# Optimization experiments

Measured on AMD Instinct MI355X. Metric: run time of the kernel, lower is better.

Reference implementation:

```python
import jax, jax.numpy as jnp
import numpy as np


def _gelu(x):
    return jax.nn.gelu(x, approximate=False)


def _mlp(g, w1, b1, w2, b2, w3, b3):
    # MLP1D: Linear(1,64) -> GELU -> Linear(64,64) -> GELU -> Linear(64,R)
    h = _gelu(g[:, None] @ w1.T + b1)
    h = _gelu(h @ w2.T + b2)
    return h @ w3.T + b3


def _forward(x,
             ah_w1, ah_b1, ah_w2, ah_b2, ah_w3, ah_b3,
             bc1_w1, bc1_b1, bc1_w2, bc1_b2, bc1_w3, bc1_b3,
             aw_w1, aw_b1, aw_w2, aw_b2, aw_w3, aw_b3,
             bc2_w1, bc2_b1, bc2_w2, bc2_b2, bc2_w3, bc2_b3,
             ca_w1, ca_b1, ca_dw, ca_db, lc_w, bn_g, bn_b, bn_m, bn_v):
    B, C, H, W = x.shape
    C2 = C // 2
    R = ah_w3.shape[0]
    xh, xw = jnp.split(x, 2, axis=1)  # (B, C2, H, W) each

    # normalized rFFT half-spectrum coordinates in [-1, 1]
    omega_h = (2.0 * jnp.pi * jnp.arange(H // 2 + 1, dtype=jnp.float32) / H) / jnp.pi - 1.0
    omega_w = (2.0 * jnp.pi * jnp.arange(W // 2 + 1, dtype=jnp.float32) / W) / jnp.pi - 1.0
    lam = jnp.linspace(-1.0, 1.0, C2, dtype=jnp.float32)

    # outer-product gates (band=None -> no mask)
    Ah = _mlp(omega_h, ah_w1, ah_b1, ah_w2, ah_b2, ah_w3, ah_b3)      # (Hh, R)
    Bh = _mlp(lam, bc1_w1, bc1_b1, bc1_w2, bc1_b2, bc1_w3, bc1_b3)    # (C2, R)
    Gh = jax.nn.softplus(jnp.einsum('hr,cr->hc', Ah, Bh)) / jnp.sqrt(jnp.float32(R))
    Aw = _mlp(omega_w, aw_w1, aw_b1, aw_w2, aw_b2, aw_w3, aw_b3)      # (Wh, R)
    Bw = _mlp(lam, bc2_w1, bc2_b1, bc2_w2, bc2_b2, bc2_w3, bc2_b3)    # (C2, R)
    Gw = jax.nn.softplus(jnp.einsum('wr,cr->wc', Aw, Bw)) / jnp.sqrt(jnp.float32(R))

    # HC branch: rFFT along H, gate (C2, Hh), irFFT (ChannelBasis is identity)
    zh = jnp.fft.rfft(xh, axis=2, norm='ortho') * Gh.T[None, :, :, None]
    yh = jnp.fft.irfft(zh, n=H, axis=2, norm='ortho')
    # WC branch: rFFT along W, gate (C2, Wh)
    zw = jnp.fft.rfft(xw, axis=3, norm='ortho') * Gw.T[None, :, None, :]
    yw = jnp.fft.irfft(zw, n=W, axis=3, norm='ortho')
    y = jnp.concatenate([yh, yw], axis=1)  # (B, C, H, W)

    # ChannelAttentionBlock: gap -> 1x1 conv -> GELU -> dw 3x3 -> sigmoid * y
    p = jnp.mean(y, axis=(2, 3))                        # (B, C)
    p = _gelu(p @ ca_w1.T + ca_b1)
    # depthwise 3x3 with padding=1 on a 1x1 spatial map == center tap only
    p = p * ca_dw[:, 1, 1][None, :] + ca_db[None, :]
    y = jax.nn.sigmoid(p)[:, :, None, None] * y

    # SimpleConv: 1x1 conv (no bias) -> BatchNorm (eval) -> GELU
    y = jnp.einsum('oc,bchw->bohw', lc_w, y)
    inv = bn_g / jnp.sqrt(bn_v + 1e-5)
    y = _gelu(y * inv[None, :, None, None] + (bn_b - bn_m * inv)[None, :, None, None])
    return x + y


def setup_inputs() -> dict:
    key = jax.random.key(0)
    ks = iter(jax.random.split(key, 48))
    B, C, H, W = 4, 256, 256, 256
    R, HID = 8, 64

    def lin(o, i):
        return jax.random.normal(next(ks), (o, i), jnp.float32) / np.sqrt(i).astype(np.float32)

    def vec(n):
        return jax.random.normal(next(ks), (n,), jnp.float32) * 0.02

    d = {"x": jax.random.normal(next(ks), (B, C, H, W), jnp.float32)}
    for name in ["ah", "bc1", "aw", "bc2"]:
        d[f"{name}_w1"] = lin(HID, 1)
        d[f"{name}_b1"] = vec(HID)
        d[f"{name}_w2"] = lin(HID, HID)
        d[f"{name}_b2"] = vec(HID)
        d[f"{name}_w3"] = lin(R, HID)
        d[f"{name}_b3"] = vec(R)
    d["ca_w1"] = lin(C, C)
    d["ca_b1"] = vec(C)
    d["ca_dw"] = jax.random.normal(next(ks), (C, 3, 3), jnp.float32) / 3.0
    d["ca_db"] = vec(C)
    d["lc_w"] = lin(C, C)
    d["bn_g"] = jnp.ones((C,), jnp.float32)
    d["bn_b"] = jnp.zeros((C,), jnp.float32)
    d["bn_m"] = vec(C)
    d["bn_v"] = jnp.ones((C,), jnp.float32)
    return d


def reference(x,
              ah_w1, ah_b1, ah_w2, ah_b2, ah_w3, ah_b3,
              bc1_w1, bc1_b1, bc1_w2, bc1_b2, bc1_w3, bc1_b3,
              aw_w1, aw_b1, aw_w2, aw_b2, aw_w3, aw_b3,
              bc2_w1, bc2_b1, bc2_w2, bc2_b2, bc2_w3, bc2_b3,
              ca_w1, ca_b1, ca_dw, ca_db, lc_w, bn_g, bn_b, bn_m, bn_v):
    return _forward(x,
                    ah_w1, ah_b1, ah_w2, ah_b2, ah_w3, ah_b3,
                    bc1_w1, bc1_b1, bc1_w2, bc1_b2, bc1_w3, bc1_b3,
                    aw_w1, aw_b1, aw_w2, aw_b2, aw_w3, aw_b3,
                    bc2_w1, bc2_b1, bc2_w2, bc2_b2, bc2_w3, bc2_b3,
                    ca_w1, ca_b1, ca_dw, ca_db, lc_w, bn_g, bn_b, bn_m, bn_v)
```

## Files before the change

### kernel.cpp

```cpp
#include <hip/hip_runtime.h>
#include <math.h>

#define DEV __device__ __forceinline__

typedef __attribute__((ext_vector_type(8))) short short8;
typedef __attribute__((ext_vector_type(4))) float floatx4;
typedef unsigned int u32;
typedef unsigned short u16;

DEV float gelu_f(float v) { return 0.5f * v * (1.0f + erff(v * 0.70710678118654752f)); }
DEV float softplus_f(float v) { return v > 15.0f ? v : log1pf(expf(v)); }

DEV u16 f2bf(float v) {
    u32 u = __float_as_uint(v);
    return (u16)((u + 0x7fffu + ((u >> 16) & 1u)) >> 16);
}

DEV void gload_lds16(const void* g, void* l) {
    __builtin_amdgcn_global_load_lds((const __attribute__((address_space(1))) u32*)g,
                                     (__attribute__((address_space(3))) u32*)l, 16, 0, 0);
}

#define WS_A(j)     ((j) * 1040)
#define WS_KBUF     4160
#define WS_P        (4160 + 65536)
#define WS_S        (WS_P + 1024)
#define Y0_B        286976u
#define AW0_B       134504704u
#define CIRC0_B     135028992u
#define XB0_B       168583424u
#define YT0_B       135028992u

struct MlpW { const float *w1, *b1, *w2, *b2, *w3, *b3; };

__global__ void mlp_kernel(MlpW a0, MlpW a1, MlpW a2, MlpW a3, float* ws) {
    int j = blockIdx.x;
    MlpW m = (j == 0) ? a0 : (j == 1) ? a1 : (j == 2) ? a2 : a3;
    int n = (j == 1 || j == 3) ? 128 : 129;
    int i = threadIdx.x;
    if (i >= n) return;
    float g;
    if (j == 1 || j == 3) g = -1.0f + 2.0f * i / 127.0f;
    else                  g = 2.0f * i / 256.0f - 1.0f;
    float h1[64], h2[64];
    for (int k = 0; k < 64; k++) h1[k] = gelu_f(g * m.w1[k] + m.b1[k]);
    for (int q = 0; q < 64; q++) {
        float acc = m.b2[q];
        for (int k = 0; k < 64; k++) acc += h1[k] * m.w2[q * 64 + k];
        h2[q] = gelu_f(acc);
    }
    float* outp = ws + WS_A(j) + i * 8;
    for (int r = 0; r < 8; r++) {
        float acc = m.b3[r];
        for (int k = 0; k < 64; k++) acc += h2[k] * m.w3[r * 64 + k];
        outp[r] = acc;
    }
}

__global__ void gatek_kernel(float* ws) {
    int br = blockIdx.x >> 7, c = blockIdx.x & 127;
    const float* A = ws + WS_A(br == 0 ? 0 : 2);
    const float* B = ws + WS_A(br == 0 ? 1 : 3);
    __shared__ float G[129];
    int t = threadIdx.x;
    if (t < 129) {
        float acc = 0.f;
        for (int r = 0; r < 8; r++) acc += A[t * 8 + r] * B[c * 8 + r];
        G[t] = softplus_f(acc) * 0.35355339059327373f;
    }
    __syncthreads();
    float g0 = G[0], g128 = G[128];
    float acc = g0 + ((t & 1) ? -g128 : g128);
    for (int f = 1; f < 128; f++) {
        int idx = (f * t) & 255;
        acc += 2.0f * G[f] * cosf(idx * 0.02454369260617026f);
    }
    ws[WS_KBUF + blockIdx.x * 256 + t] = acc * (1.0f / 256.0f);
}

__global__ void circmat(const float* __restrict__ ws, u16* __restrict__ circ) {
    int mi = blockIdx.x, t = threadIdx.x;
    __shared__ float kl[256];
    kl[t] = ws[WS_KBUF + mi * 256 + t];
    __syncthreads();
    u16* M = circ + (size_t)mi * 65536u;
    for (int it = 0; it < 32; it++) {
        int e = it * 2048 + t * 8;
        int i = e >> 8, j = e & 255;
        u16 tmp[8];
#pragma unroll
        for (int jj = 0; jj < 8; jj++) tmp[jj] = f2bf(kl[(i - j - jj) & 255]);
        *(uint4*)&M[e] = *(uint4*)tmp;
    }
}

__global__ void prep(const float* __restrict__ x, u16* __restrict__ xb) {
    int tile = blockIdx.x;
    int mat = blockIdx.y;
    int t = threadIdx.x;
    const float* xm = x + (size_t)mat * 65536u;
    u16* xo = xb + (size_t)mat * 65536u;
    __shared__ float lt[64][65];
    if ((mat & 255) >= 128) {
        int base = tile * 4096 + t * 16;
#pragma unroll
        for (int q = 0; q < 4; q++) {
            float4 v = *(const float4*)&xm[base + q * 4];
            ushort4 o; o.x = f2bf(v.x); o.y = f2bf(v.y); o.z = f2bf(v.z); o.w = f2bf(v.w);
            *(ushort4*)&xo[base + q * 4] = o;
        }
    } else {
        int w0 = (tile & 3) * 64, h0 = (tile >> 2) * 64;
        int rh = t >> 2, cc = (t & 3) * 16;
#pragma unroll
        for (int q = 0; q < 4; q++) {
            float4 v = *(const float4*)&xm[(h0 + rh) * 256 + w0 + cc + q * 4];
            lt[rh][cc + q * 4 + 0] = v.x; lt[rh][cc + q * 4 + 1] = v.y;
            lt[rh][cc + q * 4 + 2] = v.z; lt[rh][cc + q * 4 + 3] = v.w;
        }
        __syncthreads();
        u16 tmp[16];
#pragma unroll
        for (int j = 0; j < 16; j++) tmp[j] = f2bf(lt[cc + j][rh]);
#pragma unroll
        for (int q = 0; q < 4; q++)
            *(ushort4*)&xo[(w0 + rh) * 256 + h0 + cc + q * 4] = *(ushort4*)&tmp[q * 4];
    }
}

__global__ __launch_bounds__(256) void gate_gemm(
    const u16* __restrict__ xb, const u16* __restrict__ circ,
    u16* __restrict__ y, float* __restrict__ ws)
{
    const int tile = blockIdx.x, c = blockIdx.y, zb = blockIdx.z;
    const int b = zb >> 1, br = zb & 1;
    const int m0 = (tile >> 1) * 128, n0 = (tile & 1) * 128;
    const int t = threadIdx.x, lane = t & 63, w = t >> 6;
    const int ch = br * 128 + c;

    const u16* Mbase = circ + (size_t)ch * 65536u;
    const u16* Xbase = xb + (size_t)(b * 256 + ch) * 65536u;
    const int rM0 = br ? n0 : m0;
    const int rX0 = br ? m0 : n0;

    __shared__ u16 ldsM[4096];
    __shared__ u16 ldsX[4096];

    const int s1 = t + 256;
    const int kq0 = t >> 7, r0s = t & 127;
    const int kq1 = s1 >> 7, r1s = s1 & 127;
    const u16* gM0 = Mbase + (rM0 + r0s) * 256 + kq0 * 8;
    const u16* gM1 = Mbase + (rM0 + r1s) * 256 + kq1 * 8;
    const u16* gX0 = Xbase + (rX0 + r0s) * 256 + kq0 * 8;
    const u16* gX1 = Xbase + (rX0 + r1s) * 256 + kq1 * 8;
    u16* lM0 = &ldsM[(t & 192) * 8];
    u16* lM1 = &ldsM[((t & 192) + 256) * 8];
    u16* lX0 = &ldsX[(t & 192) * 8];
    u16* lX1 = &ldsX[((t & 192) + 256) * 8];

    floatx4 acc[4][4];
#pragma unroll
    for (int i = 0; i < 4; i++)
#pragma unroll
        for (int j = 0; j < 4; j++) acc[i][j] = (floatx4){0.f, 0.f, 0.f, 0.f};

    const int wm = (w & 1) * 64, wn = (w >> 1) * 64;
    const int fr = lane & 15, fq = lane >> 4;
    const u16* aB = br ? ldsX : ldsM;
    const u16* bB = br ? ldsM : ldsX;

    for (int k0 = 0; k0 < 256; k0 += 32) {
        gload_lds16(gM0, lM0); gload_lds16(gM1, lM1);
        gload_lds16(gX0, lX0); gload_lds16(gX1, lX1);
        gM0 += 32; gM1 += 32; gX0 += 32; gX1 += 32;
        __syncthreads();
        short8 aF[4], bF[4];
#pragma unroll
        for (int i = 0; i < 4; i++) aF[i] = *(const short8*)&aB[(fq * 128 + wm + i * 16 + fr) * 8];
#pragma unroll
        for (int j = 0; j < 4; j++) bF[j] = *(const short8*)&bB[(fq * 128 + wn + j * 16 + fr) * 8];
#pragma unroll
        for (int i = 0; i < 4; i++)
#pragma unroll
            for (int j = 0; j < 4; j++)
                acc[i][j] = __builtin_amdgcn_mfma_f32_16x16x32_bf16(aF[i], bF[j], acc[i][j], 0, 0, 0);
        __syncthreads();
    }

    size_t ybase = (size_t)(b * 256 + ch) * 65536u;
    float lsum = 0.f;
#pragma unroll
    for (int i = 0; i < 4; i++)
#pragma unroll
        for (int r = 0; r < 4; r++) {
            int row = m0 + wm + i * 16 + fq * 4 + r;
            size_t rb = ybase + (size_t)row * 256;
#pragma unroll
            for (int j = 0; j < 4; j++) {
                float v = acc[i][j][r];
                lsum += v;
                y[rb + n0 + wn + j * 16 + fr] = f2bf(v);
            }
        }
    for (int off = 32; off; off >>= 1) lsum += __shfl_down(lsum, off, 64);
    __shared__ float wsum[4];
    if (lane == 0) wsum[w] = lsum;
    __syncthreads();
    if (t == 0) atomicAdd(ws + WS_P + b * 256 + ch, wsum[0] + wsum[1] + wsum[2] + wsum[3]);
}

__global__ void attn_kernel(const float* __restrict__ ca_w1, const float* __restrict__ ca_b1,
                            const float* __restrict__ ca_dw, const float* __restrict__ ca_db,
                            const float* __restrict__ lc_w, float* ws, u16* __restrict__ aw) {
    int b = blockIdx.x, o = threadIdx.x;
    __shared__ float pm[256];
    __shared__ float sl[256];
    pm[o] = ws[WS_P + b * 256 + o] * (1.0f / 65536.0f);
    __syncthreads();
    float acc = ca_b1[o];
    for (int c2 = 0; c2 < 256; c2++) acc += ca_w1[o * 256 + c2] * pm[c2];
    float q = gelu_f(acc);
    float tv = q * ca_dw[o * 9 + 4] + ca_db[o];
    float s = 1.0f / (1.0f + expf(-tv));
    ws[WS_S + b * 256 + o] = s;
    sl[o] = s;
    __syncthreads();
    u16* awb = aw + b * 65536;
    for (int row = 0; row < 256; row++)
        awb[row * 256 + o] = f2bf(lc_w[row * 256 + o] * sl[o]);
}

__global__ void ytrans(const u16* __restrict__ y, u16* __restrict__ yt) {
    int pt = blockIdx.x, ct = blockIdx.y, b = blockIdx.z;
    const u16* yb = y + (size_t)b * 16777216u;
    u16* ytb = yt + (size_t)b * 16777216u;
    int p0 = pt * 64, c0 = ct * 64;
    __shared__ u16 lt[64][74];
    int t = threadIdx.x;
    int rr = t >> 3, pc = (t & 7) * 8;
#pragma unroll
    for (int it = 0; it < 2; it++) {
        int row = rr + it * 32;
        ushort4 a0 = *(const ushort4*)&yb[(size_t)(c0 + row) * 65536u + p0 + pc];
        ushort4 a1 = *(const ushort4*)&yb[(size_t)(c0 + row) * 65536u + p0 + pc + 4];
        lt[row][pc + 0] = a0.x; lt[row][pc + 1] = a0.y; lt[row][pc + 2] = a0.z; lt[row][pc + 3] = a0.w;
        lt[row][pc + 4] = a1.x; lt[row][pc + 5] = a1.y; lt[row][pc + 6] = a1.z; lt[row][pc + 7] = a1.w;
    }
    __syncthreads();
#pragma unroll
    for (int it = 0; it < 2; it++) {
        int row = rr + it * 32;
        u16 tmp[8];
#pragma unroll
        for (int j = 0; j < 8; j++) tmp[j] = lt[pc + j][row];
        *(uint4*)&ytb[(size_t)(p0 + row) * 256 + c0 + pc] = *(uint4*)tmp;
    }
}

__global__ __launch_bounds__(256) void conv_gemm(
    const float* __restrict__ x, const u16* __restrict__ aw, const u16* __restrict__ yt,
    const float* __restrict__ bn_g, const float* __restrict__ bn_b,
    const float* __restrict__ bn_m, const float* __restrict__ bn_v,
    float* __restrict__ out)
{
    const int m0 = blockIdx.x * 128;
    const int n0 = blockIdx.y * 128;
    const int b = blockIdx.z;
    const int t = threadIdx.x, lane = t & 63, w = t >> 6;

    const u16* Abase = aw + (size_t)b * 65536u;
    const u16* Bbase = yt + (size_t)b * 16777216u;

    __shared__ u16 ldsA[4096];
    __shared__ u16 ldsB[4096];

    const int s1 = t + 256;
    const int kq0 = t >> 7, r0s = t & 127;
    const int kq1 = s1 >> 7, r1s = s1 & 127;
    const u16* gA0 = Abase + (m0 + r0s) * 256 + kq0 * 8;
    const u16* gA1 = Abase + (m0 + r1s) * 256 + kq1 * 8;
    const u16* gB0 = Bbase + (size_t)(n0 + r0s) * 256 + kq0 * 8;
    const u16* gB1 = Bbase + (size_t)(n0 + r1s) * 256 + kq1 * 8;
    u16* lA0 = &ldsA[(t & 192) * 8];
    u16* lA1 = &ldsA[((t & 192) + 256) * 8];
    u16* lB0 = &ldsB[(t & 192) * 8];
    u16* lB1 = &ldsB[((t & 192) + 256) * 8];

    floatx4 acc[4][4];
#pragma unroll
    for (int i = 0; i < 4; i++)
#pragma unroll
        for (int j = 0; j < 4; j++) acc[i][j] = (floatx4){0.f, 0.f, 0.f, 0.f};

    const int wm = (w & 1) * 64, wn = (w >> 1) * 64;
    const int fr = lane & 15, fq = lane >> 4;

    for (int k0 = 0; k0 < 256; k0 += 32) {
        gload_lds16(gA0, lA0); gload_lds16(gA1, lA1);
        gload_lds16(gB0, lB0); gload_lds16(gB1, lB1);
        gA0 += 32; gA1 += 32; gB0 += 32; gB1 += 32;
        __syncthreads();
        short8 aF[4], bF[4];
#pragma unroll
        for (int i = 0; i < 4; i++) aF[i] = *(const short8*)&ldsA[(fq * 128 + wm + i * 16 + fr) * 8];
#pragma unroll
        for (int j = 0; j < 4; j++) bF[j] = *(const short8*)&ldsB[(fq * 128 + wn + j * 16 + fr) * 8];
#pragma unroll
        for (int i = 0; i < 4; i++)
#pragma unroll
            for (int j = 0; j < 4; j++)
                acc[i][j] = __builtin_amdgcn_mfma_f32_16x16x32_bf16(aF[i], bF[j], acc[i][j], 0, 0, 0);
        __syncthreads();
    }

#pragma unroll
    for (int i = 0; i < 4; i++)
#pragma unroll
        for (int r = 0; r < 4; r++) {
            int o = m0 + wm + i * 16 + fq * 4 + r;
            float inv = bn_g[o] * rsqrtf(bn_v[o] + 1e-5f);
            float beta = bn_b[o] - bn_m[o] * inv;
            size_t rowb = (size_t)(b * 256 + o) * 65536u;
#pragma unroll
            for (int j = 0; j < 4; j++) {
                int p = n0 + wn + j * 16 + fr;
                float v = acc[i][j][r];
                out[rowb + p] = x[rowb + p] + gelu_f(v * inv + beta);
            }
        }
}

extern "C" void kernel_launch(void* const* d_in, const int* in_sizes, int n_in,
                              void* d_out, int out_size, void* d_ws, size_t ws_size,
                              hipStream_t stream) {
    const float* x = (const float*)d_in[0];
    MlpW m[4];
    for (int j = 0; j < 4; j++) {
        m[j].w1 = (const float*)d_in[1 + 6 * j + 0];
        m[j].b1 = (const float*)d_in[1 + 6 * j + 1];
        m[j].w2 = (const float*)d_in[1 + 6 * j + 2];
        m[j].b2 = (const float*)d_in[1 + 6 * j + 3];
        m[j].w3 = (const float*)d_in[1 + 6 * j + 4];
        m[j].b3 = (const float*)d_in[1 + 6 * j + 5];
    }
    const float* ca_w1 = (const float*)d_in[25];
    const float* ca_b1 = (const float*)d_in[26];
    const float* ca_dw = (const float*)d_in[27];
    const float* ca_db = (const float*)d_in[28];
    const float* lc_w  = (const float*)d_in[29];
    const float* bn_g  = (const float*)d_in[30];
    const float* bn_b  = (const float*)d_in[31];
    const float* bn_m  = (const float*)d_in[32];
    const float* bn_v  = (const float*)d_in[33];

    char* wsb = (char*)d_ws;
    float* ws = (float*)d_ws;
    u16* ybf  = (u16*)(wsb + Y0_B);
    u16* aw   = (u16*)(wsb + AW0_B);
    u16* circ = (u16*)(wsb + CIRC0_B);
    u16* xbb  = (u16*)(wsb + XB0_B);
    u16* yt   = (u16*)(wsb + YT0_B);
    float* out = (float*)d_out;

    hipLaunchKernelGGL(mlp_kernel, dim3(4), dim3(256), 0, stream, m[0], m[1], m[2], m[3], ws);
    hipLaunchKernelGGL(gatek_kernel, dim3(256), dim3(256), 0, stream, ws);
    hipLaunchKernelGGL(circmat, dim3(256), dim3(256), 0, stream, ws, circ);
    hipLaunchKernelGGL(prep, dim3(16, 1024), dim3(256), 0, stream, x, xbb);
    hipMemsetAsync(ws + WS_P, 0, 1024 * sizeof(float), stream);
    hipLaunchKernelGGL(gate_gemm, dim3(4, 128, 8), dim3(256), 0, stream, xbb, circ, ybf, ws);
    hipLaunchKernelGGL(attn_kernel, dim3(4), dim3(256), 0, stream,
                       ca_w1, ca_b1, ca_dw, ca_db, lc_w, ws, aw);
    hipLaunchKernelGGL(ytrans, dim3(1024, 4, 4), dim3(256), 0, stream, ybf, yt);
    hipLaunchKernelGGL(conv_gemm, dim3(2, 512, 4), dim3(256), 0, stream,
                       x, aw, yt, bn_g, bn_b, bn_m, bn_v, out);
}
```

Baseline: 1.084 ms.

## Double-buffer LDS in gate and conv GEMMs to overlap loads with MFMA

Both GEMM kernels now use two LDS buffers per operand, so the global-to-LDS loads for the next K slice are issued while MFMAs run on the current slice. Plain __syncthreads are replaced with explicit vmcnt waits plus s_barrier. This hides global load latency at the cost of doubling LDS use to 32KB per block, which may lower occupancy. Correctness depends on the hand-written waitcnt counts and on the barrier after each compute stopping the buffer from being overwritten too early.

```diff
diff --git a/kernel.cpp b/kernel.cpp
--- a/kernel.cpp
+++ b/kernel.cpp
@@ -143,8 +143,8 @@
     const int rM0 = br ? n0 : m0;
     const int rX0 = br ? m0 : n0;
 
-    __shared__ u16 ldsM[4096];
-    __shared__ u16 ldsX[4096];
+    __shared__ u16 ldsM[2][4096];
+    __shared__ u16 ldsX[2][4096];
 
     const int s1 = t + 256;
     const int kq0 = t >> 7, r0s = t & 127;
@@ -153,10 +153,7 @@
     const u16* gM1 = Mbase + (rM0 + r1s) * 256 + kq1 * 8;
     const u16* gX0 = Xbase + (rX0 + r0s) * 256 + kq0 * 8;
     const u16* gX1 = Xbase + (rX0 + r1s) * 256 + kq1 * 8;
-    u16* lM0 = &ldsM[(t & 192) * 8];
-    u16* lM1 = &ldsM[((t & 192) + 256) * 8];
-    u16* lX0 = &ldsX[(t & 192) * 8];
-    u16* lX1 = &ldsX[((t & 192) + 256) * 8];
+    const int ldst = (t & 192) * 8;
 
     floatx4 acc[4][4];
 #pragma unroll
@@ -166,25 +163,44 @@
 
     const int wm = (w & 1) * 64, wn = (w >> 1) * 64;
     const int fr = lane & 15, fq = lane >> 4;
-    const u16* aB = br ? ldsX : ldsM;
-    const u16* bB = br ? ldsM : ldsX;
-
-    for (int k0 = 0; k0 < 256; k0 += 32) {
-        gload_lds16(gM0, lM0); gload_lds16(gM1, lM1);
-        gload_lds16(gX0, lX0); gload_lds16(gX1, lX1);
+    const u16* aBuf0 = br ? &ldsX[0][0] : &ldsM[0][0];
+    const u16* bBuf0 = br ? &ldsM[0][0] : &ldsX[0][0];
+    const u16* aBuf1 = br ? &ldsX[1][0] : &ldsM[1][0];
+    const u16* bBuf1 = br ? &ldsM[1][0] : &ldsX[1][0];
+
+    auto stage = [&](u16* dM, u16* dX) {
+        gload_lds16(gM0, dM); gload_lds16(gM1, dM + 2048);
+        gload_lds16(gX0, dX); gload_lds16(gX1, dX + 2048);
         gM0 += 32; gM1 += 32; gX0 += 32; gX1 += 32;
-        __syncthreads();
+    };
+    auto compute = [&](const u16* Ab, const u16* Bb) {
         short8 aF[4], bF[4];
 #pragma unroll
-        for (int i = 0; i < 4; i++) aF[i] = *(const short8*)&aB[(fq * 128 + wm + i * 16 + fr) * 8];
-#pragma unroll
-        for (int j = 0; j < 4; j++) bF[j] = *(const short8*)&bB[(fq * 128 + wn + j * 16 + fr) * 8];
+        for (int i = 0; i < 4; i++) aF[i] = *(const short8*)&Ab[(fq * 128 + wm + i * 16 + fr) * 8];
+#pragma unroll
+        for (int j = 0; j < 4; j++) bF[j] = *(const short8*)&Bb[(fq * 128 + wn + j * 16 + fr) * 8];
 #pragma unroll
         for (int i = 0; i < 4; i++)
 #pragma unroll
             for (int j = 0; j < 4; j++)
                 acc[i][j] = __builtin_amdgcn_mfma_f32_16x16x32_bf16(aF[i], bF[j], acc[i][j], 0, 0, 0);
-        __syncthreads();
+    };
+
+    stage(&ldsM[0][ldst], &ldsX[0][ldst]);
+#pragma unroll
+    for (int kk = 0; kk < 4; kk++) {
+        stage(&ldsM[1][ldst], &ldsX[1][ldst]);
+        asm volatile("s_waitcnt vmcnt(4)\n\ts_barrier" ::: "memory");
+        compute(aBuf0, bBuf0);
+        asm volatile("s_barrier" ::: "memory");
+        if (kk < 3) {
+            stage(&ldsM[0][ldst], &ldsX[0][ldst]);
+            asm volatile("s_waitcnt vmcnt(4)\n\ts_barrier" ::: "memory");
+        } else {
+            asm volatile("s_waitcnt vmcnt(0)\n\ts_barrier" ::: "memory");
+        }
+        compute(aBuf1, bBuf1);
+        asm volatile("s_barrier" ::: "memory");
     }
 
     size_t ybase = (size_t)(b * 256 + ch) * 65536u;
@@ -271,8 +287,8 @@
     const u16* Abase = aw + (size_t)b * 65536u;
     const u16* Bbase = yt + (size_t)b * 16777216u;
 
-    __shared__ u16 ldsA[4096];
-    __shared__ u16 ldsB[4096];
+    __shared__ u16 ldsA[2][4096];
+    __shared__ u16 ldsB[2][4096];
 
     const int s1 = t + 256;
     const int kq0 = t >> 7, r0s = t & 127;
@@ -281,10 +297,7 @@
     const u16* gA1 = Abase + (m0 + r1s) * 256 + kq1 * 8;
     const u16* gB0 = Bbase + (size_t)(n0 + r0s) * 256 + kq0 * 8;
     const u16* gB1 = Bbase + (size_t)(n0 + r1s) * 256 + kq1 * 8;
-    u16* lA0 = &ldsA[(t & 192) * 8];
-    u16* lA1 = &ldsA[((t & 192) + 256) * 8];
-    u16* lB0 = &ldsB[(t & 192) * 8];
-    u16* lB1 = &ldsB[((t & 192) + 256) * 8];
+    const int ldst = (t & 192) * 8;
 
     floatx4 acc[4][4];
 #pragma unroll
@@ -295,22 +308,39 @@
     const int wm = (w & 1) * 64, wn = (w >> 1) * 64;
     const int fr = lane & 15, fq = lane >> 4;
 
-    for (int k0 = 0; k0 < 256; k0 += 32) {
-        gload_lds16(gA0, lA0); gload_lds16(gA1, lA1);
-        gload_lds16(gB0, lB0); gload_lds16(gB1, lB1);
+    auto stage = [&](u16* dA, u16* dB) {
+        gload_lds16(gA0, dA); gload_lds16(gA1, dA + 2048);
+        gload_lds16(gB0, dB); gload_lds16(gB1, dB + 2048);
         gA0 += 32; gA1 += 32; gB0 += 32; gB1 += 32;
-        __syncthreads();
+    };
+    auto compute = [&](const u16* Ab, const u16* Bb) {
         short8 aF[4], bF[4];
 #pragma unroll
-        for (int i = 0; i < 4; i++) aF[i] = *(const short8*)&ldsA[(fq * 128 + wm + i * 16 + fr) * 8];
-#pragma unroll
-        for (int j = 0; j < 4; j++) bF[j] = *(const short8*)&ldsB[(fq * 128 + wn + j * 16 + fr) * 8];
+        for (int i = 0; i < 4; i++) aF[i] = *(const short8*)&Ab[(fq * 128 + wm + i * 16 + fr) * 8];
+#pragma unroll
+        for (int j = 0; j < 4; j++) bF[j] = *(const short8*)&Bb[(fq * 128 + wn + j * 16 + fr) * 8];
 #pragma unroll
         for (int i = 0; i < 4; i++)
 #pragma unroll
             for (int j = 0; j < 4; j++)
                 acc[i][j] = __builtin_amdgcn_mfma_f32_16x16x32_bf16(aF[i], bF[j], acc[i][j], 0, 0, 0);
-        __syncthreads();
+    };
+
+    stage(&ldsA[0][ldst], &ldsB[0][ldst]);
+#pragma unroll
+    for (int kk = 0; kk < 4; kk++) {
+        stage(&ldsA[1][ldst], &ldsB[1][ldst]);
+        asm volatile("s_waitcnt vmcnt(4)\n\ts_barrier" ::: "memory");
+        compute(&ldsA[0][0], &ldsB[0][0]);
+        asm volatile("s_barrier" ::: "memory");
+        if (kk < 3) {
+            stage(&ldsA[0][ldst], &ldsB[0][ldst]);
+            asm volatile("s_waitcnt vmcnt(4)\n\ts_barrier" ::: "memory");
+        } else {
+            asm volatile("s_waitcnt vmcnt(0)\n\ts_barrier" ::: "memory");
+        }
+        compute(&ldsA[1][0], &ldsB[1][0]);
+        asm volatile("s_barrier" ::: "memory");
     }
 
 #pragma unroll
```

Result: no change. 1.096 ms (+1.1%).
